# Kernel tuning notes

Measured on AMD Instinct MI355X. Metric: run time of the kernel, lower is better.

The kernel has to match this reference:

```python
import jax, jax.numpy as jnp
import numpy as np
from jax.ops import segment_sum, segment_max

N_NODES = 100000
N_EDGES = 1600000


def _glorot(key, shape):
    fan_in, fan_out = shape[0], shape[-1]
    lim = np.sqrt(6.0 / (fan_in + fan_out))
    return jax.random.uniform(key, shape, jnp.float32, -lim, lim)


def setup_inputs() -> dict:
    key = jax.random.key(0)
    ks = jax.random.split(key, 12)
    x = jax.random.normal(ks[0], (N_NODES, 7), jnp.float32)
    edge_index = jax.random.randint(ks[1], (2, N_EDGES), 0, N_NODES, jnp.int64)
    return {
        "x": x,
        "edge_index": edge_index,
        # GCNConv(7, 32)
        "W1": _glorot(ks[2], (7, 32)), "b1": jnp.zeros((32,), jnp.float32),
        # GATConv(32, 64), heads=1
        "W2": _glorot(ks[3], (32, 64)), "a_src2": _glorot(ks[4], (64, 1))[:, 0],
        "a_dst2": _glorot(ks[5], (64, 1))[:, 0], "b2": jnp.zeros((64,), jnp.float32),
        # GCNConv(64, 128)
        "W3": _glorot(ks[6], (64, 128)), "b3": jnp.zeros((128,), jnp.float32),
        # GATConv(128, 2), heads=1
        "W4": _glorot(ks[7], (128, 2)), "a_src4": _glorot(ks[8], (2, 1))[:, 0],
        "a_dst4": _glorot(ks[9], (2, 1))[:, 0], "b4": jnp.zeros((2,), jnp.float32),
    }


def _gcn_conv(x, src, dst, W, b):
    # x' = W x; symmetric normalization with self-loops already in (src, dst)
    h = x @ W
    deg = segment_sum(jnp.ones_like(dst, dtype=h.dtype), dst, num_segments=N_NODES)
    dinv = jnp.where(deg > 0, jax.lax.rsqrt(deg), 0.0)
    norm = dinv[src] * dinv[dst]            # [E]
    msg = norm[:, None] * h[src]            # [E, C]
    return segment_sum(msg, dst, num_segments=N_NODES) + b


def _gat_conv(x, src, dst, W, a_src, a_dst, b, slope=0.2):
    h = x @ W                               # [N, C]
    alpha_src = h @ a_src                   # [N]
    alpha_dst = h @ a_dst                   # [N]
    e = alpha_src[src] + alpha_dst[dst]     # [E]
    e = jnp.where(e > 0, e, slope * e)      # leaky_relu
    # numerically-stable softmax over edges grouped by destination node
    m = segment_max(e, dst, num_segments=N_NODES)
    ex = jnp.exp(e - m[dst])
    denom = segment_sum(ex, dst, num_segments=N_NODES)
    w = ex / (denom[dst] + 1e-16)           # [E]
    out = segment_sum(w[:, None] * h[src], dst, num_segments=N_NODES)
    return out + b


def reference(x, edge_index, W1, b1, W2, a_src2, a_dst2, b2, W3, b3, W4, a_src4, a_dst4, b4):
    # add self-loops once (PyG does it per layer; identical edge set each time)
    loop = jnp.arange(N_NODES, dtype=edge_index.dtype)
    src = jnp.concatenate([edge_index[0], loop])
    dst = jnp.concatenate([edge_index[1], loop])

    h = _gcn_conv(x, src, dst, W1, b1)
    h = jax.nn.relu(h)
    h = _gat_conv(h, src, dst, W2, a_src2, a_dst2, b2)
    h = jax.nn.relu(h)
    h = _gcn_conv(h, src, dst, W3, b3)
    h = jax.nn.relu(h)
    h = _gat_conv(h, src, dst, W4, a_src4, a_dst4, b4)
    return jax.nn.log_softmax(h, axis=1)
```

## Files before the change

kernel.cpp:

```cpp
#include <hip/hip_runtime.h>
#include <hip/hip_bf16.h>

#define NN 100000
#define NE 1600000
#define NT (NN + NE)
#define NBKT 256
#define BSZ 391
#define BCAP 10240

typedef unsigned int u32;
typedef unsigned short u16;

static __device__ __forceinline__ int clampN(int s) {
    return ((unsigned)s < (unsigned)NN) ? s : 0;
}
static __device__ __forceinline__ float2 b2x2(u32 u) {
    float2 r;
    r.x = __uint_as_float((u & 0xffffu) << 16);
    r.y = __uint_as_float(u & 0xffff0000u);
    return r;
}
static __device__ __forceinline__ u16 f2bs(float f) {
    union { __hip_bfloat16 b; u16 u; } cv;
    cv.b = __float2bfloat16(f);
    return cv.u;
}
static __device__ __forceinline__ u32 pack2(float x, float y) {
    return ((u32)f2bs(y) << 16) | (u32)f2bs(x);
}
static __device__ __forceinline__ float lrelu_c(float e) {
    e = (e > 0.f) ? e : 0.2f * e;
    return fminf(e, 60.f);
}

#define FMA4(acc, s, v) { acc.x += (s)*(v).x; acc.y += (s)*(v).y; \
                          acc.z += (s)*(v).z; acc.w += (s)*(v).w; }


__global__ void __launch_bounds__(256) k_init(const float* __restrict__ W2,
                                              const float* __restrict__ a2s,
                                              const float* __restrict__ a2d,
                                              const int* __restrict__ ei,
                                              float* __restrict__ va2,
                                              float* __restrict__ vd2,
                                              int* __restrict__ flag,
                                              int* __restrict__ gcur) {
    if (blockIdx.x == 0) {
        if (threadIdx.x == 0) flag[0] = 0;
        __syncthreads();
        int nz = 0;
        for (int i = threadIdx.x; i < 4096; i += 256) nz |= ei[2 * i + 1];
        if (nz) atomicOr(flag, 1);
        if (threadIdx.x < NBKT) gcur[threadIdx.x] = 0;
    } else if (threadIdx.x < 64) {
        int t = threadIdx.x;
        if (t < 32) {
            float a = 0.f;
            for (int c = 0; c < 64; c++) a += W2[t * 64 + c] * a2s[c];
            va2[t] = a;
        } else {
            int k = t - 32;
            float a = 0.f;
            for (int c = 0; c < 64; c++) a += W2[k * 64 + c] * a2d[c];
            vd2[k] = a;
        }
    }
}


__global__ void __launch_bounds__(256) k_binA(const int* __restrict__ ei,
                                              const int* __restrict__ flag,
                                              int* __restrict__ gcur,
                                              u32* __restrict__ staging) {
    __shared__ int hist[NBKT];
    __shared__ int gbase[NBKT];
    __shared__ int cnt2[NBKT];
    int tid = threadIdx.x;
    if (tid < NBKT) hist[tid] = 0;
    __syncthreads();

    int base = blockIdx.x * 4096;
    int is32 = flag[0];
    int d[16], s[16];
    #pragma unroll
    for (int i = 0; i < 16; i++) {
        int e = base + i * 256 + tid;
        d[i] = -1;
        if (e < NE) {
            int dd, ss;
            if (is32) {
                dd = ei[NE + e];
                ss = ei[e];
            } else {
                dd = ((const int2*)ei)[NE + e].x;
                ss = ((const int2*)ei)[e].x;
            }
            if ((unsigned)dd < (unsigned)NN) { d[i] = dd; s[i] = clampN(ss); }
        } else if (e < NT) {
            d[i] = e - NE; s[i] = e - NE;
        }
        if (d[i] >= 0) atomicAdd(&hist[d[i] / BSZ], 1);
    }
    __syncthreads();
    if (tid < NBKT) {
        int c = hist[tid];
        gbase[tid] = c ? atomicAdd(&gcur[tid], c) : 0;
        cnt2[tid] = 0;
    }
    __syncthreads();
    #pragma unroll
    for (int i = 0; i < 16; i++) {
        if (d[i] >= 0) {
            int b = d[i] / BSZ;
            int pos = gbase[b] + atomicAdd(&cnt2[b], 1);
            if (pos < BCAP)
                staging[(size_t)b * BCAP + pos] =
                    ((unsigned)(d[i] - b * BSZ) << 17) | (unsigned)s[i];
        }
    }
}

__global__ void __launch_bounds__(256) k_histscan(const u32* __restrict__ staging,
                                                  const int* __restrict__ gcur,
                                                  const float* __restrict__ x,
                                                  u32* __restrict__ xpb,
                                                  int* __restrict__ rowptr,
                                                  int* __restrict__ deg,
                                                  int* __restrict__ part) {
    __shared__ int h[512];
    __shared__ int sm[256];
    int b = blockIdx.x, tid = threadIdx.x;
    h[tid] = 0; h[tid + 256] = 0;
    __syncthreads();
    int cnt = min(gcur[b], BCAP);
    const u32* st = staging + (size_t)b * BCAP;
    for (int i = tid; i < cnt; i += 256)
        atomicAdd(&h[st[i] >> 17], 1);
    __syncthreads();
    int h0 = h[2 * tid], h1 = h[2 * tid + 1];
    int pair = h0 + h1;
    sm[tid] = pair;
    __syncthreads();
    for (int off = 1; off < 256; off <<= 1) {
        int t = (tid >= off) ? sm[tid - off] : 0;
        __syncthreads();
        sm[tid] += t;
        __syncthreads();
    }
    int excl = sm[tid] - pair;
    int g0 = b * BSZ + 2 * tid;
    if (2 * tid < BSZ && g0 < NN) { rowptr[g0] = excl; deg[g0] = h0; }
    int g1 = g0 + 1;
    if (2 * tid + 1 < BSZ && g1 < NN) { rowptr[g1] = excl + h0; deg[g1] = h1; }
    if (tid == 255) part[b] = sm[255];

    for (int i = b * 256 + tid; i < NN * 4; i += NBKT * 256) {
        int n = i >> 2, c2 = i & 3;
        float f0 = x[n * 7 + 2 * c2];
        float f1 = (2 * c2 + 1 < 7) ? x[n * 7 + 2 * c2 + 1] : 0.f;
        xpb[i] = pack2(f0, f1);
    }
}

__global__ void __launch_bounds__(256) k_scat(const u32* __restrict__ staging,
                                              const int* __restrict__ gcur,
                                              const int* __restrict__ part,
                                              int* __restrict__ rowptr,
                                              const int* __restrict__ deg,
                                              float* __restrict__ dinv,
                                              int* __restrict__ col) {
    __shared__ int sm[256];
    __shared__ int cur[BSZ];
    int b = blockIdx.x, tid = threadIdx.x;
    int v = part[tid];
    sm[tid] = v;
    __syncthreads();
    for (int off = 1; off < 256; off <<= 1) {
        int t = (tid >= off) ? sm[tid - off] : 0;
        __syncthreads();
        sm[tid] += t;
        __syncthreads();
    }
    int pb = (b > 0) ? sm[b - 1] : 0;
    if (b == 0 && tid == 0) rowptr[NN] = NT;
    for (int l = tid; l < BSZ; l += 256) {
        int g = b * BSZ + l;
        if (g < NN) {
            int r = rowptr[g] + pb;
            rowptr[g] = r;
            cur[l] = r;
            int d = deg[g];
            dinv[g] = rsqrtf((float)(d > 0 ? d : 1));
        } else cur[l] = 0;
    }
    __syncthreads();
    int cnt = min(gcur[b], BCAP);
    const u32* st = staging + (size_t)b * BCAP;
    for (int i = tid; i < cnt; i += 256) {
        u32 w = st[i];
        int l = w >> 17;
        int s = w & 0x1FFFF;
        int p = atomicAdd(&cur[l], 1);
        if ((unsigned)p < (unsigned)NT) col[p] = s;
    }
}


__global__ void __launch_bounds__(256) k_l1(const u32* __restrict__ xpb,
                                            const int* __restrict__ rowptr,
                                            const int* __restrict__ col,
                                            const float* __restrict__ dinv,
                                            const float* __restrict__ W1,
                                            const float* __restrict__ b1,
                                            const float* __restrict__ va2,
                                            const float* __restrict__ vd2,
                                            u32* __restrict__ O1b,
                                            float* __restrict__ as_,
                                            float* __restrict__ ad_) {
    __shared__ float sW1[7 * 32];
    __shared__ float sb1[32], sva[32], svd[32];
    __shared__ float sT1[64 * 8];
    if (threadIdx.x < 224) sW1[threadIdx.x] = W1[threadIdx.x];
    else {
        int c = threadIdx.x - 224;
        sb1[c] = b1[c]; sva[c] = va2[c]; svd[c] = vd2[c];
    }
    __syncthreads();

    int node_l = threadIdx.x >> 2;
    int lane = threadIdx.x & 3;
    int slot = lane >> 1;
    int ck = lane & 1;
    int n = blockIdx.x * 64 + node_l;
    if (n >= NN) return;
    {
        int beg = rowptr[n], end = rowptr[n + 1];
        float a0 = 0.f, a1 = 0.f, a2 = 0.f, a3 = 0.f;
        #pragma unroll 2
        for (int e = beg + slot; e < end; e += 2) {
            int s = clampN(col[e]);
            float w = dinv[s];
            uint2 u = *(const uint2*)(xpb + (size_t)s * 4 + ck * 2);
            float2 f0 = b2x2(u.x), f1 = b2x2(u.y);
            a0 += w * f0.x; a1 += w * f0.y; a2 += w * f1.x; a3 += w * f1.y;
        }
        a0 += __shfl_xor(a0, 2, 4); a1 += __shfl_xor(a1, 2, 4);
        a2 += __shfl_xor(a2, 2, 4); a3 += __shfl_xor(a3, 2, 4);
        if (slot == 0) {
            float dn = dinv[n];
            float4 o = {a0 * dn, a1 * dn, a2 * dn, a3 * dn};
            *(float4*)&sT1[node_l * 8 + ck * 4] = o;
        }
    }
    __builtin_amdgcn_wave_barrier();
    int c8 = lane * 8;
    float4 aA = {0,0,0,0}, aB = {0,0,0,0};
    #pragma unroll
    for (int k = 0; k < 7; k++) {
        float t = sT1[node_l * 8 + k];
        float4 wva = *(const float4*)&sW1[k * 32 + c8];
        float4 wvb = *(const float4*)&sW1[k * 32 + c8 + 4];
        FMA4(aA, t, wva);
        FMA4(aB, t, wvb);
    }
    float o0 = fmaxf(aA.x + sb1[c8], 0.f);
    float o1 = fmaxf(aA.y + sb1[c8 + 1], 0.f);
    float o2 = fmaxf(aA.z + sb1[c8 + 2], 0.f);
    float o3 = fmaxf(aA.w + sb1[c8 + 3], 0.f);
    float o4 = fmaxf(aB.x + sb1[c8 + 4], 0.f);
    float o5 = fmaxf(aB.y + sb1[c8 + 5], 0.f);
    float o6 = fmaxf(aB.z + sb1[c8 + 6], 0.f);
    float o7 = fmaxf(aB.w + sb1[c8 + 7], 0.f);
    uint4 pk = {pack2(o0, o1), pack2(o2, o3), pack2(o4, o5), pack2(o6, o7)};
    *(uint4*)(O1b + (size_t)n * 16 + lane * 4) = pk;
    float vs = o0 * sva[c8] + o1 * sva[c8 + 1] + o2 * sva[c8 + 2] + o3 * sva[c8 + 3]
             + o4 * sva[c8 + 4] + o5 * sva[c8 + 5] + o6 * sva[c8 + 6] + o7 * sva[c8 + 7];
    float vd = o0 * svd[c8] + o1 * svd[c8 + 1] + o2 * svd[c8 + 2] + o3 * svd[c8 + 3]
             + o4 * svd[c8 + 4] + o5 * svd[c8 + 5] + o6 * svd[c8 + 6] + o7 * svd[c8 + 7];
    vs += __shfl_xor(vs, 1, 4); vs += __shfl_xor(vs, 2, 4);
    vd += __shfl_xor(vd, 1, 4); vd += __shfl_xor(vd, 2, 4);
    if (lane == 0) { as_[n] = vs; ad_[n] = vd; }
}


__global__ void __launch_bounds__(256) k_l2(const u32* __restrict__ O1b,
                                            const float* __restrict__ as_,
                                            const float* __restrict__ ad_,
                                            const int* __restrict__ rowptr,
                                            const int* __restrict__ col,
                                            const float* __restrict__ W2,
                                            const float* __restrict__ b2,
                                            const float* __restrict__ dinv,
                                            u32* __restrict__ O2b) {
    __shared__ float sW2[32 * 64];
    __shared__ float sT2[32 * 36];
    __shared__ float sb2[64];
    {
        const float4* g = (const float4*)W2;
        float4* s4 = (float4*)sW2;
        s4[threadIdx.x] = g[threadIdx.x];
        s4[threadIdx.x + 256] = g[threadIdx.x + 256];
    }
    if (threadIdx.x < 64) sb2[threadIdx.x] = b2[threadIdx.x];
    __syncthreads();

    int node_l = threadIdx.x >> 3;
    int l8 = threadIdx.x & 7;
    int slot = l8 >> 2;
    int ck = l8 & 3;
    int n = blockIdx.x * 32 + node_l;
    {
        int beg = rowptr[n], end = rowptr[n + 1];
        float adn = ad_[n];
        float den = 0.f;
        float a0=0.f,a1=0.f,a2=0.f,a3=0.f,a4=0.f,a5=0.f,a6=0.f,a7=0.f;
        #pragma unroll 2
        for (int e = beg + slot; e < end; e += 2) {
            int s = clampN(col[e]);
            float p = __expf(lrelu_c(as_[s] + adn));
            den += p;
            uint4 w = *(const uint4*)(O1b + (size_t)s * 16 + ck * 4);
            float2 f0 = b2x2(w.x), f1 = b2x2(w.y), f2 = b2x2(w.z), f3 = b2x2(w.w);
            a0 += p * f0.x; a1 += p * f0.y; a2 += p * f1.x; a3 += p * f1.y;
            a4 += p * f2.x; a5 += p * f2.y; a6 += p * f3.x; a7 += p * f3.y;
        }
        den += __shfl_xor(den, 4, 8);
        a0 += __shfl_xor(a0, 4, 8); a1 += __shfl_xor(a1, 4, 8);
        a2 += __shfl_xor(a2, 4, 8); a3 += __shfl_xor(a3, 4, 8);
        a4 += __shfl_xor(a4, 4, 8); a5 += __shfl_xor(a5, 4, 8);
        a6 += __shfl_xor(a6, 4, 8); a7 += __shfl_xor(a7, 4, 8);
        if (slot == 0) {
            float inv = 1.0f / (den + 1e-16f);
            float4 oA = {a0 * inv, a1 * inv, a2 * inv, a3 * inv};
            float4 oB = {a4 * inv, a5 * inv, a6 * inv, a7 * inv};
            float* dst = &sT2[node_l * 36 + ck * 8];
            *(float4*)dst = oA;
            *(float4*)(dst + 4) = oB;
        }
    }
    __builtin_amdgcn_wave_barrier();

    int grp = threadIdx.x >> 4;
    int l = threadIdx.x & 15;
    int c4 = l * 4;
    int lbase = grp * 2;

    float4 acc0 = {0,0,0,0}, acc1 = {0,0,0,0};
    #pragma unroll
    for (int k4 = 0; k4 < 8; k4++) {
        float4 t0 = *(const float4*)&sT2[(lbase + 0) * 36 + 4 * k4];
        float4 t1 = *(const float4*)&sT2[(lbase + 1) * 36 + 4 * k4];
        #pragma unroll
        for (int j = 0; j < 4; j++) {
            float4 wv = *(const float4*)&sW2[(4 * k4 + j) * 64 + c4];
            FMA4(acc0, ((const float*)&t0)[j], wv);
            FMA4(acc1, ((const float*)&t1)[j], wv);
        }
    }
    float4 bb = *(const float4*)&sb2[c4];
    int n0 = blockIdx.x * 32 + lbase;
    float d0 = dinv[n0], d1 = dinv[n0 + 1];
    {
        float o0 = fmaxf(acc0.x + bb.x, 0.f) * d0;
        float o1 = fmaxf(acc0.y + bb.y, 0.f) * d0;
        float o2 = fmaxf(acc0.z + bb.z, 0.f) * d0;
        float o3 = fmaxf(acc0.w + bb.w, 0.f) * d0;
        uint2 pk = {pack2(o0, o1), pack2(o2, o3)};
        *(uint2*)(O2b + (size_t)n0 * 32 + l * 2) = pk;
    }
    {
        float o0 = fmaxf(acc1.x + bb.x, 0.f) * d1;
        float o1 = fmaxf(acc1.y + bb.y, 0.f) * d1;
        float o2 = fmaxf(acc1.z + bb.z, 0.f) * d1;
        float o3 = fmaxf(acc1.w + bb.w, 0.f) * d1;
        uint2 pk = {pack2(o0, o1), pack2(o2, o3)};
        *(uint2*)(O2b + (size_t)(n0 + 1) * 32 + l * 2) = pk;
    }
}


__global__ void __launch_bounds__(1024, 8) k_l3(const u32* __restrict__ O2b,
                                                const int* __restrict__ rowptr,
                                                const int* __restrict__ col,
                                                const float* __restrict__ dinv,
                                                const float* __restrict__ W3,
                                                const float* __restrict__ b3,
                                                const float* __restrict__ W4,
                                                const float* __restrict__ av4s,
                                                const float* __restrict__ av4d,
                                                float4* __restrict__ h4as,
                                                float* __restrict__ ad_) {
    __shared__ float sW3[64 * 128];
    __shared__ float sT3[128 * 68];
    __shared__ float sW4[128 * 2];
    __shared__ float sb3[128];

    {
        const float4* g = (const float4*)W3;
        float4* s4 = (float4*)sW3;
        #pragma unroll
        for (int i = 0; i < 2; i++) s4[threadIdx.x + 1024 * i] = g[threadIdx.x + 1024 * i];
    }
    if (threadIdx.x < 128) {
        sb3[threadIdx.x] = b3[threadIdx.x];
        sW4[2 * threadIdx.x] = W4[2 * threadIdx.x];
        sW4[2 * threadIdx.x + 1] = W4[2 * threadIdx.x + 1];
    }
    __syncthreads();

    int w = threadIdx.x >> 6;
    int l = threadIdx.x & 63;
    int row = w * 8 + (l >> 3);
    int cl = l & 7;
    int n = blockIdx.x * 128 + row;
    if (n >= NN) return;

    {
        int beg = rowptr[n], end = rowptr[n + 1];
        float4 accA = {0,0,0,0}, accB = {0,0,0,0};
        #pragma unroll 4
        for (int e = beg; e < end; e++) {
            int s = clampN(col[e]);
            uint4 wd = *(const uint4*)(O2b + (size_t)s * 32 + cl * 4);
            float2 f0 = b2x2(wd.x), f1 = b2x2(wd.y), f2 = b2x2(wd.z), f3 = b2x2(wd.w);
            accA.x += f0.x; accA.y += f0.y; accA.z += f1.x; accA.w += f1.y;
            accB.x += f2.x; accB.y += f2.y; accB.z += f3.x; accB.w += f3.y;
        }
        float dn = dinv[n];
        accA.x *= dn; accA.y *= dn; accA.z *= dn; accA.w *= dn;
        accB.x *= dn; accB.y *= dn; accB.z *= dn; accB.w *= dn;
        float* dst = &sT3[row * 68 + cl * 8];
        *(float4*)dst = accA;
        *(float4*)(dst + 4) = accB;
    }
    __builtin_amdgcn_wave_barrier();

    const float* trow = &sT3[row * 68];
    float4 acc0 = {0,0,0,0}, acc1 = {0,0,0,0}, acc2 = {0,0,0,0}, acc3 = {0,0,0,0};
    #pragma unroll 4
    for (int k4 = 0; k4 < 16; k4++) {
        float4 t4 = *(const float4*)&trow[k4 * 4];
        #pragma unroll
        for (int j = 0; j < 4; j++) {
            float tj = ((const float*)&t4)[j];
            const float* wr = &sW3[(4 * k4 + j) * 128 + 4 * cl];
            float4 w0 = *(const float4*)&wr[0];
            float4 w1 = *(const float4*)&wr[32];
            float4 w2 = *(const float4*)&wr[64];
            float4 w3v = *(const float4*)&wr[96];
            FMA4(acc0, tj, w0);
            FMA4(acc1, tj, w1);
            FMA4(acc2, tj, w2);
            FMA4(acc3, tj, w3v);
        }
    }

    float av4s0 = av4s[0], av4s1 = av4s[1];
    float av4d0 = av4d[0], av4d1 = av4d[1];
    float p0 = 0.f, p1 = 0.f;
    #pragma unroll
    for (int q = 0; q < 4; q++) {
        float4 a = (q == 0) ? acc0 : (q == 1) ? acc1 : (q == 2) ? acc2 : acc3;
        int c = 4 * cl + 32 * q;
        float4 bb = *(const float4*)&sb3[c];
        a.x = fmaxf(a.x + bb.x, 0.f);
        a.y = fmaxf(a.y + bb.y, 0.f);
        a.z = fmaxf(a.z + bb.z, 0.f);
        a.w = fmaxf(a.w + bb.w, 0.f);
        p0 += a.x * sW4[2 * c]     + a.y * sW4[2 * (c + 1)]
            + a.z * sW4[2 * (c + 2)] + a.w * sW4[2 * (c + 3)];
        p1 += a.x * sW4[2 * c + 1]     + a.y * sW4[2 * (c + 1) + 1]
            + a.z * sW4[2 * (c + 2) + 1] + a.w * sW4[2 * (c + 3) + 1];
    }
    p0 += __shfl_xor(p0, 1, 8); p0 += __shfl_xor(p0, 2, 8); p0 += __shfl_xor(p0, 4, 8);
    p1 += __shfl_xor(p1, 1, 8); p1 += __shfl_xor(p1, 2, 8); p1 += __shfl_xor(p1, 4, 8);
    if (cl == 0) {
        float asv = p0 * av4s0 + p1 * av4s1;
        float4 pk = {p0, p1, asv, 0.f};
        h4as[n] = pk;
        ad_[n] = p0 * av4d0 + p1 * av4d1;
    }
}


__global__ void k_final(const float4* __restrict__ h4as,
                        const float* __restrict__ ad_, const int* __restrict__ rowptr,
                        const int* __restrict__ col, const float* __restrict__ b,
                        float* __restrict__ out) {
    int gid = blockIdx.x * 256 + threadIdx.x;
    int n = gid >> 2;
    if (n >= NN) return;
    int lsub = gid & 3;
    int beg = rowptr[n], end = rowptr[n + 1];
    float adn = ad_[n];
    float den = 0.f, a0 = 0.f, a1 = 0.f;
    for (int e = beg + lsub; e < end; e += 4) {
        int s = clampN(col[e]);
        float4 h = h4as[s];
        float p = __expf(lrelu_c(h.z + adn));
        den += p;
        a0 += p * h.x;
        a1 += p * h.y;
    }
    den += __shfl_xor(den, 1, 4); den += __shfl_xor(den, 2, 4);
    a0  += __shfl_xor(a0, 1, 4);  a0  += __shfl_xor(a0, 2, 4);
    a1  += __shfl_xor(a1, 1, 4);  a1  += __shfl_xor(a1, 2, 4);
    if (lsub == 0) {
        float inv = 1.0f / (den + 1e-16f);
        float v0 = a0 * inv + b[0];
        float v1 = a1 * inv + b[1];
        float mx = fmaxf(v0, v1);
        float lse = mx + logf(__expf(v0 - mx) + __expf(v1 - mx));
        float2 o = {v0 - lse, v1 - lse};
        *(float2*)(out + n * 2) = o;
    }
}

__global__ void k_sentinel(float* __restrict__ out, float v) {
    int i = blockIdx.x * 256 + threadIdx.x;
    if (i < NN * 2) out[i] = v;
}


extern "C" void kernel_launch(void* const* d_in, const int* in_sizes, int n_in,
                              void* d_out, int out_size, void* d_ws, size_t ws_size,
                              hipStream_t stream) {
    const float* x    = (const float*)d_in[0];
    const int* ei     = (const int*)d_in[1];
    const float* W1   = (const float*)d_in[2];
    const float* b1   = (const float*)d_in[3];
    const float* W2   = (const float*)d_in[4];
    const float* a2s  = (const float*)d_in[5];
    const float* a2d  = (const float*)d_in[6];
    const float* b2   = (const float*)d_in[7];
    const float* W3   = (const float*)d_in[8];
    const float* b3   = (const float*)d_in[9];
    const float* W4   = (const float*)d_in[10];
    const float* a4s  = (const float*)d_in[11];
    const float* a4d  = (const float*)d_in[12];
    const float* b4   = (const float*)d_in[13];
    float* out = (float*)d_out;

    char* base = (char*)d_ws;
    size_t off = 0;
    auto alloc = [&](size_t bytes) {
        char* q = base + off;
        off += (bytes + 255) & ~(size_t)255;
        return q;
    };
    u32* xpb     = (u32*)alloc((size_t)NN * 4 * 4);
    u32* O1b     = (u32*)alloc((size_t)NN * 16 * 4);
    u32* O2b     = (u32*)alloc((size_t)NN * 32 * 4);
    u32* staging = (u32*)alloc((size_t)NBKT * BCAP * 4);
    int* col     = (int*)alloc((size_t)NT * 4);
    int* rowptr  = (int*)alloc((size_t)(NN + 1) * 4);
    int* deg     = (int*)alloc((size_t)NN * 4);
    float* dinv  = (float*)alloc((size_t)NN * 4);
    float* as_   = (float*)alloc((size_t)NN * 4);
    float* ad_   = (float*)alloc((size_t)NN * 4);
    float4* h4as = (float4*)alloc((size_t)NN * 16);
    int* part    = (int*)alloc(512 * 4);
    int* flag    = (int*)alloc(256);
    int* gcur    = (int*)alloc(NBKT * 4);
    float* va2   = (float*)alloc(32 * 4);
    float* vd2   = (float*)alloc(32 * 4);

    float code = 0.f;
    if (off > ws_size)            code = 1000.f + (float)(ws_size >> 20);
    else if (n_in != 14)          code = 2000.f + 10.f * (float)n_in;
    else if (out_size != NN * 2)  code = 3400.f;
    if (code != 0.f) {
        k_sentinel<<<(NN * 2 + 255) / 256, 256, 0, stream>>>(out, code);
        return;
    }

    const int NTILE = (NT + 4095) / 4096;

    k_init<<<2, 256, 0, stream>>>(W2, a2s, a2d, ei, va2, vd2, flag, gcur);
    k_binA<<<NTILE, 256, 0, stream>>>(ei, flag, gcur, staging);
    k_histscan<<<NBKT, 256, 0, stream>>>(staging, gcur, x, xpb, rowptr, deg, part);
    k_scat<<<NBKT, 256, 0, stream>>>(staging, gcur, part, rowptr, deg, dinv, col);

    k_l1<<<(NN + 63) / 64, 256, 0, stream>>>(xpb, rowptr, col, dinv,
                                             W1, b1, va2, vd2, O1b, as_, ad_);
    k_l2<<<NN / 32, 256, 0, stream>>>(O1b, as_, ad_, rowptr, col,
                                      W2, b2, dinv, O2b);
    k_l3<<<(NN + 127) / 128, 1024, 0, stream>>>(O2b, rowptr, col, dinv,
                                                W3, b3, W4, a4s, a4d, h4as, ad_);
    k_final<<<NN * 4 / 256 + 1, 256, 0, stream>>>(h4as, ad_, rowptr, col, b4, out);
}
```

Before: 257.8 us.

## Process nodes in degree-sorted order and shrink layer-3 blocks to 512 threads

Builds a degree histogram while the CSR is constructed, scans it, and adds a kernel that creates a node permutation grouped by in-degree. All layer kernels then visit nodes through this permutation, so threads in a wavefront handle nodes of similar degree and lose less time to divergence. Layer 3 also moves from 1024-thread blocks of 128 nodes to 512-thread blocks of 64 nodes, which halves its shared tile. The cost is an extra kernel launch, atomics on 256 bins, an indirect node index that scatters output writes, and the loss of node-order locality for gathers.

```diff
diff --git a/kernel.cpp b/kernel.cpp
--- a/kernel.cpp
+++ b/kernel.cpp
@@ -44,9 +44,13 @@
                                               float* __restrict__ va2,
                                               float* __restrict__ vd2,
                                               int* __restrict__ flag,
-                                              int* __restrict__ gcur) {
+                                              int* __restrict__ gcur,
+                                              int* __restrict__ dbins,
+                                              int* __restrict__ dcur) {
     if (blockIdx.x == 0) {
         if (threadIdx.x == 0) flag[0] = 0;
+        dbins[threadIdx.x] = 0;
+        dcur[threadIdx.x] = 0;
         __syncthreads();
         int nz = 0;
         for (int i = threadIdx.x; i < 4096; i += 256) nz |= ei[2 * i + 1];
@@ -126,7 +130,8 @@
                                                   u32* __restrict__ xpb,
                                                   int* __restrict__ rowptr,
                                                   int* __restrict__ deg,
-                                                  int* __restrict__ part) {
+                                                  int* __restrict__ part,
+                                                  int* __restrict__ dbins) {
     __shared__ int h[512];
     __shared__ int sm[256];
     int b = blockIdx.x, tid = threadIdx.x;
@@ -149,9 +154,15 @@
     }
     int excl = sm[tid] - pair;
     int g0 = b * BSZ + 2 * tid;
-    if (2 * tid < BSZ && g0 < NN) { rowptr[g0] = excl; deg[g0] = h0; }
+    if (2 * tid < BSZ && g0 < NN) {
+        rowptr[g0] = excl; deg[g0] = h0;
+        atomicAdd(&dbins[min(h0, 255)], 1);
+    }
     int g1 = g0 + 1;
-    if (2 * tid + 1 < BSZ && g1 < NN) { rowptr[g1] = excl + h0; deg[g1] = h1; }
+    if (2 * tid + 1 < BSZ && g1 < NN) {
+        rowptr[g1] = excl + h0; deg[g1] = h1;
+        atomicAdd(&dbins[min(h1, 255)], 1);
+    }
     if (tid == 255) part[b] = sm[255];
 
     for (int i = b * 256 + tid; i < NN * 4; i += NBKT * 256) {
@@ -168,7 +179,9 @@
                                               int* __restrict__ rowptr,
                                               const int* __restrict__ deg,
                                               float* __restrict__ dinv,
-                                              int* __restrict__ col) {
+                                              int* __restrict__ col,
+                                              const int* __restrict__ dbins,
+                                              int* __restrict__ dbase) {
     __shared__ int sm[256];
     __shared__ int cur[BSZ];
     int b = blockIdx.x, tid = threadIdx.x;
@@ -203,10 +216,36 @@
         int p = atomicAdd(&cur[l], 1);
         if ((unsigned)p < (unsigned)NT) col[p] = s;
     }
+    if (b == 0) {
+        __syncthreads();
+        int dv = dbins[tid];
+        sm[tid] = dv;
+        __syncthreads();
+        for (int off = 1; off < 256; off <<= 1) {
+            int t = (tid >= off) ? sm[tid - off] : 0;
+            __syncthreads();
+            sm[tid] += t;
+            __syncthreads();
+        }
+        dbase[tid] = sm[tid] - dv;
+    }
+}
+
+__global__ void __launch_bounds__(256) k_dperm(const int* __restrict__ deg,
+                                               const int* __restrict__ dbase,
+                                               int* __restrict__ dcur,
+                                               int* __restrict__ perm) {
+    int i = blockIdx.x * 256 + threadIdx.x;
+    if (i < NN) {
+        int bb = min(deg[i], 255);
+        int pos = atomicAdd(&dcur[bb], 1);
+        perm[dbase[bb] + pos] = i;
+    }
 }
 
 
 __global__ void __launch_bounds__(256) k_l1(const u32* __restrict__ xpb,
+                                            const int* __restrict__ perm,
                                             const int* __restrict__ rowptr,
                                             const int* __restrict__ col,
                                             const float* __restrict__ dinv,
@@ -231,8 +270,9 @@
     int lane = threadIdx.x & 3;
     int slot = lane >> 1;
     int ck = lane & 1;
-    int n = blockIdx.x * 64 + node_l;
-    if (n >= NN) return;
+    int idx = blockIdx.x * 64 + node_l;
+    if (idx >= NN) return;
+    int n = perm[idx];
     {
         int beg = rowptr[n], end = rowptr[n + 1];
         float a0 = 0.f, a1 = 0.f, a2 = 0.f, a3 = 0.f;
@@ -286,6 +326,7 @@
 __global__ void __launch_bounds__(256) k_l2(const u32* __restrict__ O1b,
                                             const float* __restrict__ as_,
                                             const float* __restrict__ ad_,
+                                            const int* __restrict__ perm,
                                             const int* __restrict__ rowptr,
                                             const int* __restrict__ col,
                                             const float* __restrict__ W2,
@@ -308,7 +349,7 @@
     int l8 = threadIdx.x & 7;
     int slot = l8 >> 2;
     int ck = l8 & 3;
-    int n = blockIdx.x * 32 + node_l;
+    int n = perm[blockIdx.x * 32 + node_l];
     {
         int beg = rowptr[n], end = rowptr[n + 1];
         float adn = ad_[n];
@@ -358,8 +399,9 @@
         }
     }
     float4 bb = *(const float4*)&sb2[c4];
-    int n0 = blockIdx.x * 32 + lbase;
-    float d0 = dinv[n0], d1 = dinv[n0 + 1];
+    int n0 = perm[blockIdx.x * 32 + lbase];
+    int n1 = perm[blockIdx.x * 32 + lbase + 1];
+    float d0 = dinv[n0], d1 = dinv[n1];
     {
         float o0 = fmaxf(acc0.x + bb.x, 0.f) * d0;
         float o1 = fmaxf(acc0.y + bb.y, 0.f) * d0;
@@ -374,24 +416,25 @@
         float o2 = fmaxf(acc1.z + bb.z, 0.f) * d1;
         float o3 = fmaxf(acc1.w + bb.w, 0.f) * d1;
         uint2 pk = {pack2(o0, o1), pack2(o2, o3)};
-        *(uint2*)(O2b + (size_t)(n0 + 1) * 32 + l * 2) = pk;
-    }
-}
-
-
-__global__ void __launch_bounds__(1024, 8) k_l3(const u32* __restrict__ O2b,
-                                                const int* __restrict__ rowptr,
-                                                const int* __restrict__ col,
-                                                const float* __restrict__ dinv,
-                                                const float* __restrict__ W3,
-                                                const float* __restrict__ b3,
-                                                const float* __restrict__ W4,
-                                                const float* __restrict__ av4s,
-                                                const float* __restrict__ av4d,
-                                                float4* __restrict__ h4as,
-                                                float* __restrict__ ad_) {
+        *(uint2*)(O2b + (size_t)n1 * 32 + l * 2) = pk;
+    }
+}
+
+
+__global__ void __launch_bounds__(512) k_l3(const u32* __restrict__ O2b,
+                                            const int* __restrict__ perm,
+                                            const int* __restrict__ rowptr,
+                                            const int* __restrict__ col,
+                                            const float* __restrict__ dinv,
+                                            const float* __restrict__ W3,
+                                            const float* __restrict__ b3,
+                                            const float* __restrict__ W4,
+                                            const float* __restrict__ av4s,
+                                            const float* __restrict__ av4d,
+                                            float4* __restrict__ h4as,
+                                            float* __restrict__ ad_) {
     __shared__ float sW3[64 * 128];
-    __shared__ float sT3[128 * 68];
+    __shared__ float sT3[64 * 68];
     __shared__ float sW4[128 * 2];
     __shared__ float sb3[128];
 
@@ -399,7 +442,7 @@
         const float4* g = (const float4*)W3;
         float4* s4 = (float4*)sW3;
         #pragma unroll
-        for (int i = 0; i < 2; i++) s4[threadIdx.x + 1024 * i] = g[threadIdx.x + 1024 * i];
+        for (int i = 0; i < 4; i++) s4[threadIdx.x + 512 * i] = g[threadIdx.x + 512 * i];
     }
     if (threadIdx.x < 128) {
         sb3[threadIdx.x] = b3[threadIdx.x];
@@ -412,8 +455,9 @@
     int l = threadIdx.x & 63;
     int row = w * 8 + (l >> 3);
     int cl = l & 7;
-    int n = blockIdx.x * 128 + row;
-    if (n >= NN) return;
+    int idx = blockIdx.x * 64 + row;
+    if (idx >= NN) return;
+    int n = perm[idx];
 
     {
         int beg = rowptr[n], end = rowptr[n + 1];
@@ -484,12 +528,15 @@
 
 
 __global__ void k_final(const float4* __restrict__ h4as,
-                        const float* __restrict__ ad_, const int* __restrict__ rowptr,
+                        const float* __restrict__ ad_,
+                        const int* __restrict__ perm,
+                        const int* __restrict__ rowptr,
                         const int* __restrict__ col, const float* __restrict__ b,
                         float* __restrict__ out) {
     int gid = blockIdx.x * 256 + threadIdx.x;
-    int n = gid >> 2;
-    if (n >= NN) return;
+    int idx = gid >> 2;
+    if (idx >= NN) return;
+    int n = perm[idx];
     int lsub = gid & 3;
     int beg = rowptr[n], end = rowptr[n + 1];
     float adn = ad_[n];
@@ -559,9 +606,13 @@
     float* as_   = (float*)alloc((size_t)NN * 4);
     float* ad_   = (float*)alloc((size_t)NN * 4);
     float4* h4as = (float4*)alloc((size_t)NN * 16);
+    int* perm    = (int*)alloc((size_t)NN * 4);
     int* part    = (int*)alloc(512 * 4);
     int* flag    = (int*)alloc(256);
     int* gcur    = (int*)alloc(NBKT * 4);
+    int* dbins   = (int*)alloc(256 * 4);
+    int* dbase   = (int*)alloc(256 * 4);
+    int* dcur    = (int*)alloc(256 * 4);
     float* va2   = (float*)alloc(32 * 4);
     float* vd2   = (float*)alloc(32 * 4);
 
@@ -575,17 +626,20 @@
     }
 
     const int NTILE = (NT + 4095) / 4096;
-
-    k_init<<<2, 256, 0, stream>>>(W2, a2s, a2d, ei, va2, vd2, flag, gcur);
+    const int NPB = (NN + 255) / 256;
+
+    k_init<<<2, 256, 0, stream>>>(W2, a2s, a2d, ei, va2, vd2, flag, gcur, dbins, dcur);
     k_binA<<<NTILE, 256, 0, stream>>>(ei, flag, gcur, staging);
-    k_histscan<<<NBKT, 256, 0, stream>>>(staging, gcur, x, xpb, rowptr, deg, part);
-    k_scat<<<NBKT, 256, 0, stream>>>(staging, gcur, part, rowptr, deg, dinv, col);
-
-    k_l1<<<(NN + 63) / 64, 256, 0, stream>>>(xpb, rowptr, col, dinv,
+    k_histscan<<<NBKT, 256, 0, stream>>>(staging, gcur, x, xpb, rowptr, deg, part, dbins);
+    k_scat<<<NBKT, 256, 0, stream>>>(staging, gcur, part, rowptr, deg, dinv, col,
+                                     dbins, dbase);
+    k_dperm<<<NPB, 256, 0, stream>>>(deg, dbase, dcur, perm);
+
+    k_l1<<<(NN + 63) / 64, 256, 0, stream>>>(xpb, perm, rowptr, col, dinv,
                                              W1, b1, va2, vd2, O1b, as_, ad_);
-    k_l2<<<NN / 32, 256, 0, stream>>>(O1b, as_, ad_, rowptr, col,
+    k_l2<<<NN / 32, 256, 0, stream>>>(O1b, as_, ad_, perm, rowptr, col,
                                       W2, b2, dinv, O2b);
-    k_l3<<<(NN + 127) / 128, 1024, 0, stream>>>(O2b, rowptr, col, dinv,
-                                                W3, b3, W4, a4s, a4d, h4as, ad_);
-    k_final<<<NN * 4 / 256 + 1, 256, 0, stream>>>(h4as, ad_, rowptr, col, b4, out);
-}
+    k_l3<<<(NN + 63) / 64, 512, 0, stream>>>(O2b, perm, rowptr, col, dinv,
+                                             W3, b3, W4, a4s, a4d, h4as, ad_);
+    k_final<<<NN * 4 / 256 + 1, 256, 0, stream>>>(h4as, ad_, perm, rowptr, col, b4, out);
+}
```

Measured after the change: 811.7 us. 3.15x slower.
